# Performance work log

Measured on AMD Instinct MI355X. Metric: run time of the kernel, lower is better.

Reference implementation:

```python
import jax, jax.numpy as jnp
import numpy as np

N = 50000
NEG_SLOPE = 0.2


def _gat_layer(x, W, a_src, a_dst, b, src, dst, heads, out_dim):
    # Linear transform per head: [N, heads, out]
    h = (x @ W).reshape(N, heads, out_dim)
    # Per-node attention halves (PyG: att applied to [x_i || x_j])
    alpha_s = jnp.einsum('nho,ho->nh', h, a_src)  # source/message half
    alpha_d = jnp.einsum('nho,ho->nh', h, a_dst)  # destination half
    # Per-edge logits with leaky relu, [E, heads]
    e = jax.nn.leaky_relu(alpha_s[src] + alpha_d[dst], negative_slope=NEG_SLOPE)
    # Segment softmax over edges sharing the same destination node
    m = jax.ops.segment_max(e, dst, num_segments=N)
    m = jax.lax.stop_gradient(m)
    ex = jnp.exp(e - m[dst])
    denom = jax.ops.segment_sum(ex, dst, num_segments=N)
    coef = ex / denom[dst]                         # [E, heads]
    # Weighted scatter-aggregate of source messages
    msg = h[src] * coef[:, :, None]                # [E, heads, out]
    agg = jax.ops.segment_sum(msg, dst, num_segments=N)
    return agg.reshape(N, heads * out_dim) + b


def _add_self_loops(edge_index):
    loops = jnp.arange(N, dtype=edge_index.dtype)
    src = jnp.concatenate([edge_index[0], loops])
    dst = jnp.concatenate([edge_index[1], loops])
    return src, dst


def setup_inputs() -> dict:
    key = jax.random.key(0)
    ks = jax.random.split(key, 9)
    E = 800000
    x = jax.random.normal(ks[0], (N, 128), dtype=jnp.float32)
    edge_index = jax.random.randint(ks[1], (2, E), 0, N, dtype=jnp.int64)
    # Glorot-ish scaled params
    W1 = jax.random.normal(ks[2], (128, 64), dtype=jnp.float32) * (1.0 / np.sqrt(128))
    a1_src = jax.random.normal(ks[3], (8, 8), dtype=jnp.float32) * 0.3
    a1_dst = jax.random.normal(ks[4], (8, 8), dtype=jnp.float32) * 0.3
    b1 = jnp.zeros((64,), dtype=jnp.float32)
    W2 = jax.random.normal(ks[5], (64, 40), dtype=jnp.float32) * (1.0 / np.sqrt(64))
    a2_src = jax.random.normal(ks[6], (1, 40), dtype=jnp.float32) * 0.3
    a2_dst = jax.random.normal(ks[7], (1, 40), dtype=jnp.float32) * 0.3
    b2 = jnp.zeros((40,), dtype=jnp.float32)
    return {"x": x, "edge_index": edge_index, "W1": W1, "a1_src": a1_src,
            "a1_dst": a1_dst, "b1": b1, "W2": W2, "a2_src": a2_src,
            "a2_dst": a2_dst, "b2": b2}


def reference(x, edge_index, W1, a1_src, a1_dst, b1, W2, a2_src, a2_dst, b2):
    # Eval mode: all F.dropout(p=0.6) calls are identity.
    src, dst = _add_self_loops(edge_index)
    h = _gat_layer(x, W1, a1_src, a1_dst, b1, src, dst, heads=8, out_dim=8)
    h = jax.nn.elu(h)
    h = _gat_layer(h, W2, a2_src, a2_dst, b2, src, dst, heads=1, out_dim=40)
    return jax.nn.log_softmax(h, axis=1)
```

## Files before the change

### kernel.cpp

```cpp
#include <hip/hip_runtime.h>
#include <hip/hip_bf16.h>
#include <math.h>

#define N_NODES 50000
#define E_EDGES 800000
#define E_TOT   850000
#define NEG_SLOPE 0.2f
#define SCAN_BLOCKS 49

__global__ void k_detect(const unsigned int* __restrict__ ei, int* __restrict__ flag) {
    __shared__ int anynz;
    int t = threadIdx.x;
    if (t == 0) anynz = 0;
    __syncthreads();
    int nz = 0;
    for (int i = t; i < 2048; i += 256)
        nz |= (ei[2 * i + 1] != 0u);
    if (nz) atomicOr(&anynz, 1);
    __syncthreads();
    if (t == 0) *flag = (anynz == 0) ? 1 : 0;
}

__device__ __forceinline__ void edge_nodes(const void* ei, int is64, int e, int& s, int& d) {
    if (e >= E_EDGES) { s = d = e - E_EDGES; return; }
    if (is64) {
        const long long* p = (const long long*)ei;
        s = (int)p[e]; d = (int)p[E_EDGES + e];
    } else {
        const int* p = (const int*)ei;
        s = p[e]; d = p[E_EDGES + e];
    }
}

__global__ void k_count(const void* __restrict__ ei, const int* __restrict__ flag,
                        int* __restrict__ counts) {
    int e = blockIdx.x * 256 + threadIdx.x;
    if (e >= E_TOT) return;
    int s, d;
    edge_nodes(ei, *flag, e, s, d);
    atomicAdd(&counts[d], 1);
}

__global__ __launch_bounds__(1024) void k_scanA(int* __restrict__ offs,
                                                int* __restrict__ partials) {
    __shared__ int lds[1024];
    const int t   = threadIdx.x;
    const int idx = blockIdx.x * 1024 + t;
    int v = (idx <= N_NODES) ? offs[idx] : 0;
    lds[t] = v;
    __syncthreads();
    for (int off = 1; off < 1024; off <<= 1) {
        int u = (t >= off) ? lds[t - off] : 0;
        __syncthreads();
        lds[t] += u;
        __syncthreads();
    }
    int incl = lds[t];
    if (idx <= N_NODES) offs[idx] = incl - v;
    if (t == 1023) partials[blockIdx.x] = incl;
}

__global__ __launch_bounds__(1024) void k_scanC(int* __restrict__ offs,
                                                const int* __restrict__ partials,
                                                int* __restrict__ cursor) {
    __shared__ int sprefix;
    const int t   = threadIdx.x;
    const int bid = blockIdx.x;
    if (t < 64) {
        int p = (t < bid) ? partials[t] : 0;
#pragma unroll
        for (int off = 32; off; off >>= 1) p += __shfl_down(p, off);
        if (t == 0) sprefix = p;
    }
    __syncthreads();
    const int idx = bid * 1024 + t;
    if (idx <= N_NODES) {
        int v = offs[idx] + sprefix;
        offs[idx] = v;
        if (idx < N_NODES) cursor[idx] = v;
    }
}

__global__ void k_fill(const void* __restrict__ ei, const int* __restrict__ flag,
                       int* __restrict__ cursor, int* __restrict__ csr_src) {
    int e = blockIdx.x * 256 + threadIdx.x;
    if (e >= E_TOT) return;
    int s, d;
    edge_nodes(ei, *flag, e, s, d);
    int pos = atomicAdd(&cursor[d], 1);
    csr_src[pos] = s;
}

__global__ __launch_bounds__(256) void k1_transform(
        const float* __restrict__ x, const float* __restrict__ W1,
        const float* __restrict__ a1s, const float* __restrict__ a1d,
        float* __restrict__ h1, float* __restrict__ as1, float* __restrict__ ad1) {
    __shared__ float ws[128 * 64];
    __shared__ float xs[64 * 132];
    const int t  = threadIdx.x;
    const int nb = blockIdx.x * 64;
    for (int i = t * 4; i < 128 * 64; i += 1024)
        *(float4*)&ws[i] = *(const float4*)&W1[i];
    for (int i = t * 4; i < 64 * 128; i += 1024) {
        int n = i >> 7, k = i & 127;
        float4 v = make_float4(0.f, 0.f, 0.f, 0.f);
        if (nb + n < N_NODES) v = *(const float4*)&x[(size_t)(nb + n) * 128 + k];
        *(float4*)&xs[n * 132 + k] = v;
    }
    __syncthreads();

    const int oq = t & 15;
    const int nq = t >> 4;
    float4 acc[4];
#pragma unroll
    for (int i = 0; i < 4; ++i) acc[i] = make_float4(0.f, 0.f, 0.f, 0.f);

    for (int k = 0; k < 128; k += 4) {
        float4 wv0 = *(float4*)&ws[(k + 0) * 64 + oq * 4];
        float4 wv1 = *(float4*)&ws[(k + 1) * 64 + oq * 4];
        float4 wv2 = *(float4*)&ws[(k + 2) * 64 + oq * 4];
        float4 wv3 = *(float4*)&ws[(k + 3) * 64 + oq * 4];
#pragma unroll
        for (int i = 0; i < 4; ++i) {
            float4 xv = *(float4*)&xs[(nq * 4 + i) * 132 + k];
            acc[i].x += xv.x * wv0.x + xv.y * wv1.x + xv.z * wv2.x + xv.w * wv3.x;
            acc[i].y += xv.x * wv0.y + xv.y * wv1.y + xv.z * wv2.y + xv.w * wv3.y;
            acc[i].z += xv.x * wv0.z + xv.y * wv1.z + xv.z * wv2.z + xv.w * wv3.z;
            acc[i].w += xv.x * wv0.w + xv.y * wv1.w + xv.z * wv2.w + xv.w * wv3.w;
        }
    }
    __syncthreads();
#pragma unroll
    for (int i = 0; i < 4; ++i) {
        int n = nq * 4 + i;
        *(float4*)&xs[n * 68 + oq * 4] = acc[i];
        if (nb + n < N_NODES)
            *(float4*)&h1[(size_t)(nb + n) * 64 + oq * 4] = acc[i];
    }
    __syncthreads();
    for (int p = t; p < 512; p += 256) {
        int n = p >> 3, hd = p & 7;
        float ss = 0.f, dd = 0.f;
#pragma unroll
        for (int o = 0; o < 8; ++o) {
            float hv = xs[n * 68 + hd * 8 + o];
            ss += hv * a1s[hd * 8 + o];
            dd += hv * a1d[hd * 8 + o];
        }
        if (nb + n < N_NODES) {
            as1[(nb + n) * 8 + hd] = ss;
            ad1[(nb + n) * 8 + hd] = dd;
        }
    }
}

__global__ __launch_bounds__(256) void k_agg1f(
        const float* __restrict__ h1, const float* __restrict__ as1g,
        const float* __restrict__ ad1g, const int* __restrict__ offs,
        const int* __restrict__ csr, const float* __restrict__ b1,
        const float* __restrict__ W2, const float* __restrict__ a2s,
        const float* __restrict__ a2d,
        float* __restrict__ h2p, float* __restrict__ as2, float* __restrict__ ad2) {
    __shared__ float ws[64 * 40];
    __shared__ float rows[4][64];
    const int t = threadIdx.x;
    for (int i = t; i < 64 * 40; i += 256) ws[i] = W2[i];
    __syncthreads();

    const int w = t >> 6, l = t & 63;
    const int wid = blockIdx.x * 4 + w;
    if (wid >= N_NODES) return;
    const int hd = l >> 3;
    const float ad = ad1g[wid * 8 + hd];
    const int j0 = offs[wid], j1 = offs[wid + 1];
    const int j1m = j1 - 1;

    float acc = 0.f, den = 0.f;
    int c[8];
#pragma unroll
    for (int i = 0; i < 8; ++i) c[i] = csr[min(j0 + i, j1m)];
    for (int j = j0; j < j1; ) {
        int s[8];
#pragma unroll
        for (int i = 0; i < 8; ++i) s[i] = c[i];
        const int rem = j1 - j;
        j += 8;
        if (j < j1) {
#pragma unroll
            for (int i = 0; i < 8; ++i) c[i] = csr[min(j + i, j1m)];
        }
        float a[8], g[8];
#pragma unroll
        for (int i = 0; i < 8; ++i) a[i] = as1g[s[i] * 8 + hd];
#pragma unroll
        for (int i = 0; i < 8; ++i) g[i] = h1[(size_t)s[i] * 64 + l];
#pragma unroll
        for (int i = 0; i < 8; ++i) {
            float e = a[i] + ad;
            e = (e > 0.f) ? e : NEG_SLOPE * e;
            float xp = (i < rem) ? __expf(e) : 0.f;
            den += xp;
            acc = fmaf(xp, g[i], acc);
        }
    }

    float v = acc / den + b1[l];
    v = (v > 0.f) ? v : expm1f(v);
    rows[w][l] = v;

    float acc2 = 0.f;
    if (l < 40) {
#pragma unroll 8
        for (int k = 0; k < 64; ++k)
            acc2 = fmaf(rows[w][k], ws[k * 40 + l], acc2);
    }
    float ps = (l < 40) ? acc2 * a2s[l] : 0.f;
    float pd = (l < 40) ? acc2 * a2d[l] : 0.f;
#pragma unroll
    for (int off = 32; off; off >>= 1) {
        ps += __shfl_down(ps, off);
        pd += __shfl_down(pd, off);
    }
    if (l < 40) h2p[(size_t)wid * 48 + l] = acc2;
    if (l == 0) { as2[wid] = ps; ad2[wid] = pd; }
}

__global__ __launch_bounds__(256) void k_agg2(
        const float* __restrict__ h2p, const float* __restrict__ as2,
        const float* __restrict__ ad2, const int* __restrict__ offs,
        const int* __restrict__ csr, const float* __restrict__ b2,
        float* __restrict__ out) {
    int wid = (blockIdx.x * 256 + threadIdx.x) >> 6;
    int l   = threadIdx.x & 63;
    if (wid >= N_NODES) return;
    const bool act = (l < 40);
    const float ad = ad2[wid];
    const int j0 = offs[wid], j1 = offs[wid + 1];
    const int j1m = j1 - 1;

    float acc = 0.f, den = 0.f;
    int c[8];
#pragma unroll
    for (int i = 0; i < 8; ++i) c[i] = csr[min(j0 + i, j1m)];
    for (int j = j0; j < j1; ) {
        int s[8];
#pragma unroll
        for (int i = 0; i < 8; ++i) s[i] = c[i];
        const int rem = j1 - j;
        j += 8;
        if (j < j1) {
#pragma unroll
            for (int i = 0; i < 8; ++i) c[i] = csr[min(j + i, j1m)];
        }
        float a[8], g[8];
#pragma unroll
        for (int i = 0; i < 8; ++i) a[i] = as2[s[i]];
#pragma unroll
        for (int i = 0; i < 8; ++i) g[i] = act ? h2p[(size_t)s[i] * 48 + l] : 0.f;
#pragma unroll
        for (int i = 0; i < 8; ++i) {
            float e = a[i] + ad;
            e = (e > 0.f) ? e : NEG_SLOPE * e;
            float xp = (i < rem) ? __expf(e) : 0.f;
            den += xp;
            acc = fmaf(xp, g[i], acc);
        }
    }

    float v = act ? (acc / den + b2[l]) : -1e30f;
    float m = v;
#pragma unroll
    for (int off = 32; off; off >>= 1) m = fmaxf(m, __shfl_xor(m, off));
    float ex2 = act ? __expf(v - m) : 0.f;
    float s2 = ex2;
#pragma unroll
    for (int off = 32; off; off >>= 1) s2 += __shfl_xor(s2, off);
    if (act) out[(size_t)wid * 40 + l] = v - m - __logf(s2);
}

extern "C" void kernel_launch(void* const* d_in, const int* in_sizes, int n_in,
                              void* d_out, int out_size, void* d_ws, size_t ws_size,
                              hipStream_t stream) {
    const float* x   = (const float*)d_in[0];
    const void*  ei  = d_in[1];
    const float* W1  = (const float*)d_in[2];
    const float* a1s = (const float*)d_in[3];
    const float* a1d = (const float*)d_in[4];
    const float* b1  = (const float*)d_in[5];
    const float* W2  = (const float*)d_in[6];
    const float* a2s = (const float*)d_in[7];
    const float* a2d = (const float*)d_in[8];
    const float* b2  = (const float*)d_in[9];
    float* out = (float*)d_out;

    float* fws = (float*)d_ws;
    float* h1  = fws + 0;
    float* as1 = fws + 3200000;
    float* ad1 = fws + 3600000;
    float* h2p = fws + 4000000;
    float* as2 = fws + 6400000;
    float* ad2 = fws + 6450000;
    int*   offs     = (int*)(fws + 6500000);
    int*   cursor   = offs + (N_NODES + 1);
    int*   csr      = cursor + N_NODES;
    int*   flag     = csr + E_TOT;
    int*   partials = flag + 1;

    hipMemsetAsync(offs, 0, (N_NODES + 1) * sizeof(int), stream);

    k_detect<<<1, 256, 0, stream>>>((const unsigned int*)ei, flag);

    int egrid = (E_TOT + 255) / 256;
    k_count<<<egrid, 256, 0, stream>>>(ei, flag, offs);
    k_scanA<<<SCAN_BLOCKS, 1024, 0, stream>>>(offs, partials);
    k_scanC<<<SCAN_BLOCKS, 1024, 0, stream>>>(offs, partials, cursor);
    k_fill<<<egrid, 256, 0, stream>>>(ei, flag, cursor, csr);

    k1_transform<<<(N_NODES + 63) / 64, 256, 0, stream>>>(x, W1, a1s, a1d, h1, as1, ad1);

    int ngrid = (N_NODES + 3) / 4;
    k_agg1f<<<ngrid, 256, 0, stream>>>(h1, as1, ad1, offs, csr, b1,
                                       W2, a2s, a2d, h2p, as2, ad2);
    k_agg2<<<ngrid, 256, 0, stream>>>(h2p, as2, ad2, offs, csr, b2, out);
}
```

Measured before the change: 316.9 us.

## Fuse memset into detect kernel and streamline aggregation edge loops

Replaces the separate hipMemsetAsync and single-block detect kernel with one multi-block kernel that zeroes offsets and detects index width, removing one launch. The aggregation loops split into a full-chunk main loop without per-element bounds masks plus a masked tail, padding the CSR array with zeroed entries so prefetch reads past the segment end stay safe. Offsets are made wave-uniform via readfirstlane, 32-bit index arithmetic replaces size_t, and leaky-relu becomes fmaxf. The changes cut scalar/vector overhead in the gather loops at the cost of a reworked workspace layout.

Result: faster. 300.2 us (-5.3%).

```diff
diff --git a/kernel.cpp b/kernel.cpp
--- a/kernel.cpp
+++ b/kernel.cpp
@@ -8,17 +8,22 @@
 #define NEG_SLOPE 0.2f
 #define SCAN_BLOCKS 49
 
-__global__ void k_detect(const unsigned int* __restrict__ ei, int* __restrict__ flag) {
-    __shared__ int anynz;
-    int t = threadIdx.x;
-    if (t == 0) anynz = 0;
-    __syncthreads();
-    int nz = 0;
-    for (int i = t; i < 2048; i += 256)
-        nz |= (ei[2 * i + 1] != 0u);
-    if (nz) atomicOr(&anynz, 1);
-    __syncthreads();
-    if (t == 0) *flag = (anynz == 0) ? 1 : 0;
+__global__ __launch_bounds__(256) void k_detect0(const unsigned int* __restrict__ ei,
+                                                 int* __restrict__ flag,
+                                                 int* __restrict__ offs) {
+    int gid = blockIdx.x * 256 + threadIdx.x;
+    for (int i = gid; i <= N_NODES; i += gridDim.x * 256) offs[i] = 0;
+    if (blockIdx.x == 0) {
+        __shared__ int anynz;
+        if (threadIdx.x == 0) anynz = 0;
+        __syncthreads();
+        int nz = 0;
+        for (int i = threadIdx.x; i < 2048; i += 256)
+            nz |= (ei[2 * i + 1] != 0u);
+        if (nz) atomicOr(&anynz, 1);
+        __syncthreads();
+        if (threadIdx.x == 0) *flag = (anynz == 0) ? 1 : 0;
+    }
 }
 
 __device__ __forceinline__ void edge_nodes(const void* ei, int is64, int e, int& s, int& d) {
@@ -84,6 +89,7 @@
 __global__ void k_fill(const void* __restrict__ ei, const int* __restrict__ flag,
                        int* __restrict__ cursor, int* __restrict__ csr_src) {
     int e = blockIdx.x * 256 + threadIdx.x;
+    if (e < 16) csr_src[E_TOT + e] = 0;
     if (e >= E_TOT) return;
     int s, d;
     edge_nodes(ei, *flag, e, s, d);
@@ -172,32 +178,46 @@
     if (wid >= N_NODES) return;
     const int hd = l >> 3;
     const float ad = ad1g[wid * 8 + hd];
-    const int j0 = offs[wid], j1 = offs[wid + 1];
-    const int j1m = j1 - 1;
+    const int j0 = __builtin_amdgcn_readfirstlane(offs[wid]);
+    const int j1 = __builtin_amdgcn_readfirstlane(offs[wid + 1]);
 
     float acc = 0.f, den = 0.f;
     int c[8];
 #pragma unroll
-    for (int i = 0; i < 8; ++i) c[i] = csr[min(j0 + i, j1m)];
-    for (int j = j0; j < j1; ) {
+    for (int i = 0; i < 8; ++i) c[i] = csr[j0 + i];
+    int j = j0;
+    while (j + 8 <= j1) {
         int s[8];
 #pragma unroll
         for (int i = 0; i < 8; ++i) s[i] = c[i];
-        const int rem = j1 - j;
-        j += 8;
-        if (j < j1) {
-#pragma unroll
-            for (int i = 0; i < 8; ++i) c[i] = csr[min(j + i, j1m)];
-        }
+#pragma unroll
+        for (int i = 0; i < 8; ++i) c[i] = csr[j + 8 + i];
         float a[8], g[8];
 #pragma unroll
-        for (int i = 0; i < 8; ++i) a[i] = as1g[s[i] * 8 + hd];
-#pragma unroll
-        for (int i = 0; i < 8; ++i) g[i] = h1[(size_t)s[i] * 64 + l];
+        for (int i = 0; i < 8; ++i) a[i] = as1g[(unsigned)s[i] * 8u + (unsigned)hd];
+#pragma unroll
+        for (int i = 0; i < 8; ++i) g[i] = h1[(unsigned)s[i] * 64u + (unsigned)l];
 #pragma unroll
         for (int i = 0; i < 8; ++i) {
             float e = a[i] + ad;
-            e = (e > 0.f) ? e : NEG_SLOPE * e;
+            e = fmaxf(e, NEG_SLOPE * e);
+            float xp = __expf(e);
+            den += xp;
+            acc = fmaf(xp, g[i], acc);
+        }
+        j += 8;
+    }
+    const int rem = j1 - j;
+    if (rem) {
+        float a[8], g[8];
+#pragma unroll
+        for (int i = 0; i < 8; ++i) a[i] = as1g[(unsigned)c[i] * 8u + (unsigned)hd];
+#pragma unroll
+        for (int i = 0; i < 8; ++i) g[i] = h1[(unsigned)c[i] * 64u + (unsigned)l];
+#pragma unroll
+        for (int i = 0; i < 8; ++i) {
+            float e = a[i] + ad;
+            e = fmaxf(e, NEG_SLOPE * e);
             float xp = (i < rem) ? __expf(e) : 0.f;
             den += xp;
             acc = fmaf(xp, g[i], acc);
@@ -221,7 +241,7 @@
         ps += __shfl_down(ps, off);
         pd += __shfl_down(pd, off);
     }
-    if (l < 40) h2p[(size_t)wid * 48 + l] = acc2;
+    if (l < 40) h2p[(unsigned)wid * 48u + (unsigned)l] = acc2;
     if (l == 0) { as2[wid] = ps; ad2[wid] = pd; }
 }
 
@@ -235,32 +255,46 @@
     if (wid >= N_NODES) return;
     const bool act = (l < 40);
     const float ad = ad2[wid];
-    const int j0 = offs[wid], j1 = offs[wid + 1];
-    const int j1m = j1 - 1;
+    const int j0 = __builtin_amdgcn_readfirstlane(offs[wid]);
+    const int j1 = __builtin_amdgcn_readfirstlane(offs[wid + 1]);
 
     float acc = 0.f, den = 0.f;
     int c[8];
 #pragma unroll
-    for (int i = 0; i < 8; ++i) c[i] = csr[min(j0 + i, j1m)];
-    for (int j = j0; j < j1; ) {
+    for (int i = 0; i < 8; ++i) c[i] = csr[j0 + i];
+    int j = j0;
+    while (j + 8 <= j1) {
         int s[8];
 #pragma unroll
         for (int i = 0; i < 8; ++i) s[i] = c[i];
-        const int rem = j1 - j;
-        j += 8;
-        if (j < j1) {
-#pragma unroll
-            for (int i = 0; i < 8; ++i) c[i] = csr[min(j + i, j1m)];
-        }
+#pragma unroll
+        for (int i = 0; i < 8; ++i) c[i] = csr[j + 8 + i];
         float a[8], g[8];
 #pragma unroll
         for (int i = 0; i < 8; ++i) a[i] = as2[s[i]];
 #pragma unroll
-        for (int i = 0; i < 8; ++i) g[i] = act ? h2p[(size_t)s[i] * 48 + l] : 0.f;
+        for (int i = 0; i < 8; ++i) g[i] = act ? h2p[(unsigned)s[i] * 48u + (unsigned)l] : 0.f;
 #pragma unroll
         for (int i = 0; i < 8; ++i) {
             float e = a[i] + ad;
-            e = (e > 0.f) ? e : NEG_SLOPE * e;
+            e = fmaxf(e, NEG_SLOPE * e);
+            float xp = __expf(e);
+            den += xp;
+            acc = fmaf(xp, g[i], acc);
+        }
+        j += 8;
+    }
+    const int rem = j1 - j;
+    if (rem) {
+        float a[8], g[8];
+#pragma unroll
+        for (int i = 0; i < 8; ++i) a[i] = as2[c[i]];
+#pragma unroll
+        for (int i = 0; i < 8; ++i) g[i] = act ? h2p[(unsigned)c[i] * 48u + (unsigned)l] : 0.f;
+#pragma unroll
+        for (int i = 0; i < 8; ++i) {
+            float e = a[i] + ad;
+            e = fmaxf(e, NEG_SLOPE * e);
             float xp = (i < rem) ? __expf(e) : 0.f;
             den += xp;
             acc = fmaf(xp, g[i], acc);
@@ -303,12 +337,10 @@
     int*   offs     = (int*)(fws + 6500000);
     int*   cursor   = offs + (N_NODES + 1);
     int*   csr      = cursor + N_NODES;
-    int*   flag     = csr + E_TOT;
-    int*   partials = flag + 1;
-
-    hipMemsetAsync(offs, 0, (N_NODES + 1) * sizeof(int), stream);
-
-    k_detect<<<1, 256, 0, stream>>>((const unsigned int*)ei, flag);
+    int*   partials = csr + E_TOT + 16;
+    int*   flag     = partials + SCAN_BLOCKS;
+
+    k_detect0<<<64, 256, 0, stream>>>((const unsigned int*)ei, flag, offs);
 
     int egrid = (E_TOT + 255) / 256;
     k_count<<<egrid, 256, 0, stream>>>(ei, flag, offs);
```
